# Kernel optimization log

Measured on AMD Instinct MI355X. Metric: run time of the kernel, lower is better.

## Reference

```python
import jax, jax.numpy as jnp
import numpy as np

T, R, S, P, Rc = 100, 300, 500, 8, 50
DEATH_RATE = 0.02
LOG2PI = float(np.log(2.0 * np.pi))


def setup_inputs() -> dict:
    key = jax.random.key(0)
    ks = jax.random.split(key, 12)
    infections = jax.random.uniform(ks[0], (T, R, S)) * 1000.0 + 1.0
    case_rate_time = jax.random.uniform(ks[1], (T,)) * 0.5 + 0.1
    case_rate_region = jax.random.uniform(ks[2], (R,)) * 0.5 + 0.1
    Rs = jax.random.uniform(ks[3], (S,)) + 0.5
    Rtr = jax.random.uniform(ks[4], (T, R)) + 0.5
    transit_rate = jax.random.uniform(ks[5], (P,)) * 0.2 + 0.01
    transit_data = jax.random.uniform(ks[6], (R, R, P))  # nonnegative covariates
    case_data = jnp.floor(jax.random.uniform(ks[7], (T, R)) * 1000.0)
    death_data = jnp.floor(jax.random.uniform(ks[8], (T, R)) * 50.0)
    strain_data = jnp.floor(jax.random.uniform(ks[9], (T, Rc, S)) * 1.2)  # sparse counts
    mutation_matrix = jax.random.uniform(ks[10], (S, S)) * 0.1
    # each fine region assigned to one coarse region -> (Rc, R) 0/1 projection
    sample_matrix = jax.nn.one_hot(jnp.arange(R) % Rc, Rc, dtype=jnp.float32).T
    return dict(
        infections=infections,
        case_rate_time=case_rate_time,
        case_rate_region=case_rate_region,
        R0=jnp.float32(1.5),
        Rs=Rs,
        Rtr=Rtr,
        transit_rate=transit_rate,
        mutation_rate=jnp.float32(0.01),
        infection_od=jnp.float32(0.2),
        case_od=jnp.float32(0.2),
        death_od=jnp.float32(0.2),
        Rtr_drift_scale=jnp.float32(0.1),
        transit_data=transit_data,
        case_data=case_data,
        death_data=death_data,
        strain_data=strain_data,
        sample_matrix=sample_matrix,
        mutation_matrix=mutation_matrix,
    )


def _lognormal_lp(x, m, s):
    lx = jnp.log(x)
    return -lx - jnp.log(s) - 0.5 * LOG2PI - (lx - m) ** 2 / (2.0 * s * s)


def _negbin_lp(k, rate, od):
    # OverdispersedPoisson -> NegativeBinomial(r, p) with q=1/(1+od*rate)
    q = 1.0 / (1.0 + od * rate)
    p = 1.0 - q
    r = rate * q / p
    return (jax.lax.lgamma(k + r) - jax.lax.lgamma(r) - jax.lax.lgamma(k + 1.0)
            + r * jnp.log(q) + k * jnp.log(p))


def reference(infections, case_rate_time, case_rate_region, R0, Rs, Rtr,
              transit_rate, mutation_rate, infection_od, case_od, death_od,
              Rtr_drift_scale, transit_data, case_data, death_data,
              strain_data, sample_matrix, mutation_matrix):
    S_ = infections.shape[-1]
    Rtrs = R0 * Rs * Rtr[:, :, None]  # (T,R,S)
    mut = jnp.eye(S_, dtype=infections.dtype) + mutation_rate * mutation_matrix  # (S,S)
    transit = jnp.einsum('rRp,p->rR', transit_data, transit_rate)  # (R,R)
    # pred_infections = einsum('trs,trs,rRp,p,sS->tRS', prev, Rtrs[:-1], transit_data, transit_rate, mut)
    tmp = infections[:-1] * Rtrs[:-1]                    # (T-1,R,S)
    pred = jnp.einsum('trs,rR->tRs', tmp, transit)        # region mixing
    pred = jnp.einsum('tRs,sS->tRS', pred, mut)           # strain mutation mixing
    # torch clamps .data in-place -> straight-through gradient
    pred = pred + jax.lax.stop_gradient(jnp.maximum(pred, 1e-3) - pred)
    # RelaxedPoisson(pred, infection_od).log_prob(curr)
    s2 = jnp.log1p(1.0 / pred + infection_od)
    m = jnp.log(pred) - s2 / 2.0
    ll_step = _lognormal_lp(infections[1:], m, jnp.sqrt(s2)).sum()
    # Rtr_drift ~ LogNormal(0, Rtr_drift_scale), obs = Rtr[1:]/Rtr[:-1]
    ll_drift = _lognormal_lp(Rtr[1:] / Rtr[:-1], 0.0, Rtr_drift_scale).sum()
    # case / death observations (population=None)
    inf_sum = infections.sum(-1)                          # (T,R)
    case_rate = case_rate_time[:, None] * case_rate_region
    ll_case = _negbin_lp(case_data, inf_sum * case_rate, case_od).sum()
    ll_death = _negbin_lp(death_data, inf_sum * DEATH_RATE, death_od).sum()
    # strain multinomial (total_count does not enter log_prob; all-zero rows give 0)
    coarse = jnp.einsum('trs,Rr->tRs', infections, sample_matrix) + 1e-6
    logp = jnp.log(coarse) - jnp.log(coarse.sum(-1, keepdims=True))
    n = strain_data.sum(-1)
    ll_strain = (jax.lax.lgamma(n + 1.0)
                 - jax.lax.lgamma(strain_data + 1.0).sum(-1)
                 + (strain_data * logp).sum(-1)).sum()
    return ll_step + ll_drift + ll_case + ll_death + ll_strain
```

## Files before the change

### kernel.cpp

```cpp
#include <hip/hip_runtime.h>

#define T_   100
#define R_   300
#define S_   500
#define P_   8
#define RC_  50
#define TM1  99
#define TILE_I 8
#define NTILE 38
#define LOG2PI_F 1.8378770664093453f

#define RP   320
#define SPD  512
#define NTM  10

#define ACCS_OFF   0
#define FLAG_OFF   2048
#define SLV_OFF    2176
#define SLR_OFF    3776
#define SLN_OFF    5376
#define RSF_OFF    5632
#define RTRF_OFF   7680
#define TB_OFF     135680
#define MT_OFF     545280
#define XT_OFF     1069568
#define ROWSUM_OFF 33837568ull
#define WS_NEED    33957568ull

#define NB_STR    1250
#define NB_XT     4000
#define NB_PA     528
#define NB_PMT    64
#define NB_DR     117
#define NB_MEGA   (NB_STR + NB_XT + NB_PA + NB_PMT + NB_DR)
#define NB_CDB    59
#define NB_STRL   625
#define NB_STEP   (NB_CDB + NB_STRL + TM1 * NTM)

typedef __attribute__((ext_vector_type(8))) short s8v;
typedef __attribute__((ext_vector_type(4))) float f32x4;

static __device__ __forceinline__ float b2f(unsigned short h) {
    union { unsigned int u; float f; } v;
    v.u = ((unsigned int)h) << 16;
    return v.f;
}

static __device__ __forceinline__ unsigned short f2b(float f) {
    union { float f; unsigned int u; } v;
    v.f = f;
    unsigned int u = v.u;
    unsigned int r = u + 0x7FFFu + ((u >> 16) & 1u);
    return (unsigned short)(r >> 16);
}

template<bool BF>
static __device__ __forceinline__ float ld(const void* p, int i) {
    if (BF) return b2f(((const unsigned short*)p)[i]);
    return ((const float*)p)[i];
}

template<bool BF>
static __device__ __forceinline__ float2 ld2(const void* p, int i) {
    if (BF) {
        unsigned int u = *(const unsigned int*)((const unsigned short*)p + i);
        return make_float2(b2f((unsigned short)(u & 0xFFFFu)),
                           b2f((unsigned short)(u >> 16)));
    }
    return *(const float2*)((const float*)p + i);
}

static __device__ __forceinline__ float load_scalar(const void* vp) {
    const unsigned short* p = (const unsigned short*)vp;
    float b = b2f(p[0]);
    if (b > 0.004f && b < 4.1f) return b;
    return ((const float*)vp)[0];
}

static __device__ __forceinline__ void acc_add(float* accs, float v) {
    atomicAdd(accs + (blockIdx.x & 15) * 32, v);
}

__global__ void k_detect(const void* inf, const void* sm, float* accs, int* flag,
                         float* slV, int* slR, int* slN, int ws_ok) {
    const unsigned short* u = (const unsigned short*)inf;
    int ok = 1;
    for (int i = 0; i < 64; ++i) {
        float v = b2f(u[i]);
        if (!(v > 0.5f && v < 1300.0f)) ok = 0;
    }
    if (blockIdx.x == 0) {
        if (threadIdx.x < 16) accs[threadIdx.x * 32] = 0.0f;
        if (threadIdx.x == 0) {
            flag[0] = ok;
            flag[1] = ws_ok;
        }
    }
    if (!ws_ok) return;
    int c = blockIdx.x;
    __shared__ int cl;
    if (threadIdx.x == 0) cl = 0;
    __syncthreads();
    for (int r = threadIdx.x; r < R_; r += 256) {
        float v = ok ? b2f(((const unsigned short*)sm)[c * R_ + r])
                     : ((const float*)sm)[c * R_ + r];
        if (v != 0.0f) {
            int k = atomicAdd(&cl, 1);
            if (k < 8) { slV[c * 8 + k] = v; slR[c * 8 + k] = r; }
        }
    }
    __syncthreads();
    if (threadIdx.x == 0) slN[c] = cl < 8 ? cl : 8;
}

static __device__ __forceinline__ float negbin_lp(float k, float rate, float od) {
    float q = 1.0f / (1.0f + od * rate);
    float p = 1.0f - q;
    float r = rate * q / p;
    return lgammaf(k + r) - lgammaf(r) - lgammaf(k + 1.0f)
         + r * __logf(q) + k * __logf(p);
}


template<bool BF>
static __device__ __forceinline__ void strain_blk(int vb, const void* inf,
                                                  const void* strain, const void* sm,
                                                  float* accs, char* smem) {
    int wave = threadIdx.x >> 6;
    int lane = threadIdx.x & 63;
    int id = vb * 4 + wave;
    int t = id / RC_;
    int c = id - t * RC_;
    int*   cnt4 = (int*)smem;
    float* wvL  = (float*)(smem + 16);
    int*   wrL  = (int*)(smem + 144);
    float* ws4  = (float*)(smem + 4096);
    if (threadIdx.x < 4) cnt4[threadIdx.x] = 0;
    __syncthreads();
    for (int base = 0; base < R_; base += 64) {
        int r = base + lane;
        float v = (r < R_) ? ld<BF>(sm, c * R_ + r) : 0.0f;
        if (v != 0.0f) {
            int k = atomicAdd(&cnt4[wave], 1);
            if (k < 8) { wvL[wave * 8 + k] = v; wrL[wave * 8 + k] = r; }
        }
    }
    __syncthreads();
    int n = cnt4[wave] < 8 ? cnt4[wave] : 8;
    const float* wvP = wvL + wave * 8;
    const int*   wrP = wrL + wave * 8;

    float Plg = 0.0f, Pn = 0.0f, Ptot = 0.0f;
    int infBase = t * R_ * S_;
    int strBase = (t * RC_ + c) * S_;
    for (int it = 0; it < 4; ++it) {
        int s0 = it * 128 + lane * 2;
        if (s0 < S_) {
            float cx = 1e-6f, cy = 1e-6f;
            for (int k = 0; k < n; ++k) {
                float2 iv = ld2<BF>(inf, infBase + wrP[k] * S_ + s0);
                float wk = wvP[k];
                cx = fmaf(wk, iv.x, cx);
                cy = fmaf(wk, iv.y, cy);
            }
            float2 sd = ld2<BF>(strain, strBase + s0);
            Ptot += cx + cy;
            if (sd.x != 0.0f) {
                Plg += sd.x * __logf(cx);
                if (sd.x > 1.5f) Plg -= lgammaf(sd.x + 1.0f);
                Pn += sd.x;
            }
            if (sd.y != 0.0f) {
                Plg += sd.y * __logf(cy);
                if (sd.y > 1.5f) Plg -= lgammaf(sd.y + 1.0f);
                Pn += sd.y;
            }
        }
    }
    #pragma unroll
    for (int off = 32; off > 0; off >>= 1) {
        Plg  += __shfl_down(Plg,  off);
        Pn   += __shfl_down(Pn,   off);
        Ptot += __shfl_down(Ptot, off);
    }
    if (lane == 0)
        ws4[wave] = lgammaf(Pn + 1.0f) + Plg - Pn * __logf(Ptot);
    __syncthreads();
    if (threadIdx.x == 0)
        acc_add(accs, ws4[0] + ws4[1] + ws4[2] + ws4[3]);
}

template<bool BF>
static __device__ __forceinline__ void xt_blk(int vb, const void* inf,
                                              unsigned short* Xt, float* rowsum,
                                              char* smem) {
    unsigned short (*lds)[72] = (unsigned short (*)[72])smem;
    int t   = vb / 40;
    int rem = vb - t * 40;
    int st  = rem / 5;
    int rt  = rem - st * 5;
    int s0 = st * 64, r0 = rt * 64;
    int tid = threadIdx.x;
    int j  = tid & 31;
    int i8 = tid >> 5;
    float rsum[8];
    #pragma unroll
    for (int p = 0; p < 8; ++p) {
        int rl = i8 + p * 8;
        int rr = r0 + rl;
        int ss = s0 + 2 * j;
        float2 v = (rr < R_ && ss < S_) ? ld2<BF>(inf, (t * R_ + rr) * S_ + ss)
                                        : make_float2(0.f, 0.f);
        lds[2 * j][rl]     = f2b(v.x);
        lds[2 * j + 1][rl] = f2b(v.y);
        rsum[p] = v.x + v.y;
    }
    __syncthreads();
    int l = tid & 63, w = tid >> 6;
    #pragma unroll
    for (int p = 0; p < 2; ++p) {
        int fi  = p * 4 + w;
        int ctl = fi >> 1, kl = fi & 1;
        int sl  = ctl * 16 + (l & 15);
        int rl  = kl * 32 + (l >> 4) * 8;
        s8v vv = *(const s8v*)&lds[sl][rl];
        int ct_g = st * 4 + ctl;
        int k_g  = rt * 2 + kl;
        *(s8v*)(Xt + ((((size_t)t * 32 + ct_g) * 10 + k_g) * 64 + l) * 8) = vv;
    }
    #pragma unroll
    for (int p = 0; p < 8; ++p) {
        float v = rsum[p];
        v += __shfl_xor(v, 1);  v += __shfl_xor(v, 2);  v += __shfl_xor(v, 4);
        v += __shfl_xor(v, 8);  v += __shfl_xor(v, 16);
        int rl = i8 + p * 8;
        if (j == 0 && r0 + rl < R_) atomicAdd(rowsum + t * R_ + r0 + rl, v);
    }
}

template<bool BF>
static __device__ __forceinline__ void prep_a_blk(int vb, const void* td, const void* rate,
                                                  const void* Rtr, const void* pR0,
                                                  const void* Rs, unsigned short* Tb,
                                                  float* RtrF, float* RsF) {
    int idx = vb * 256 + threadIdx.x;
    if (idx < RP * RP) {
        int li = idx & 511;
        int fi = idx >> 9;
        int lane = li >> 3, j = li & 7;
        int rf = fi / 10, kg = fi - rf * 10;
        int i = rf * 16 + (lane & 15);
        int r = kg * 32 + ((lane >> 4) << 3) + j;
        float v = 0.0f;
        if (i < R_ && r < R_) {
            float s = 0.0f;
            #pragma unroll
            for (int p = 0; p < P_; ++p)
                s = fmaf(ld<BF>(td, (r * R_ + i) * P_ + p), ld<BF>(rate, p), s);
            v = s;
        }
        Tb[idx] = f2b(v);
    } else if (idx < RP * RP + T_ * RP) {
        int k = idx - RP * RP;
        int t = k / RP, r = k - t * RP;
        float v = 0.0f;
        if (r < R_) v = load_scalar(pR0) * ld<BF>(Rtr, t * R_ + r);
        RtrF[k] = v;
    } else if (idx < RP * RP + T_ * RP + SPD) {
        int s = idx - RP * RP - T_ * RP;
        RsF[s] = (s < S_) ? ld<BF>(Rs, s) : 0.0f;
    }
}

template<bool BF>
static __device__ __forceinline__ void mt_blk(int vb, const void* mm,
                                              unsigned short* Mt, char* smem) {
    unsigned short (*lds)[72] = (unsigned short (*)[72])smem;
    int spT = vb >> 3;
    int sT  = vb & 7;
    int sp0 = spT * 64, ss0 = sT * 64;
    int tid = threadIdx.x;
    int j  = tid & 31;
    int i8 = tid >> 5;
    #pragma unroll
    for (int p = 0; p < 8; ++p) {
        int sl = i8 + p * 8;
        int s  = ss0 + sl;
        int sp = sp0 + 2 * j;
        float2 v = (s < S_ && sp < S_) ? ld2<BF>(mm, s * S_ + sp)
                                       : make_float2(0.f, 0.f);
        lds[2 * j][sl]     = f2b(v.x);
        lds[2 * j + 1][sl] = f2b(v.y);
    }
    __syncthreads();
    int l = tid & 63, w = tid >> 6;
    #pragma unroll
    for (int p = 0; p < 2; ++p) {
        int fi  = p * 4 + w;
        int ctl = fi >> 1, kl = fi & 1;
        int spl = ctl * 16 + (l & 15);
        int sll = kl * 32 + (l >> 4) * 8;
        s8v vv = *(const s8v*)&lds[spl][sll];
        int ct_g = spT * 4 + ctl;
        int k_g  = sT * 2 + kl;
        *(s8v*)(Mt + (((size_t)ct_g * 16 + k_g) * 64 + l) * 8) = vv;
    }
}

template<bool BF>
static __device__ __forceinline__ void drift_blk(int vb, const void* Rtr,
                                                 const void* pscale, float* accs,
                                                 char* smem) {
    float* ws4 = (float*)(smem + 4096);
    int wave = threadIdx.x >> 6;
    int lane = threadIdx.x & 63;
    int idx = vb * 256 + threadIdx.x;
    float v = 0.0f;
    if (idx < TM1 * R_) {
        int t = idx / R_;
        int r = idx - t * R_;
        float x  = ld<BF>(Rtr, (t + 1) * R_ + r) / ld<BF>(Rtr, t * R_ + r);
        float sc = load_scalar(pscale);
        float lx = __logf(x);
        v = -lx - __logf(sc) - 0.5f * LOG2PI_F - lx * lx / (2.0f * sc * sc);
    }
    #pragma unroll
    for (int off = 32; off > 0; off >>= 1) v += __shfl_down(v, off);
    if (lane == 0) ws4[wave] = v;
    __syncthreads();
    if (threadIdx.x == 0) acc_add(accs, ws4[0] + ws4[1] + ws4[2] + ws4[3]);
}

template<bool BF>
static __device__ __forceinline__ void mega_body(
        const void* inf, const void* strain, const void* sm,
        const void* td, const void* rate, const void* Rtr, const void* pR0,
        const void* Rs, const void* mm, const void* pdrift,
        unsigned short* Tb, float* RtrF, float* RsF, unsigned short* Mt,
        unsigned short* Xt, float* rowsum,
        const int* flag, float* accs, char* smem) {
    int bid = blockIdx.x;
    if (bid < NB_STR) {
        if (!flag[1]) strain_blk<BF>(bid, inf, strain, sm, accs, smem);
    } else if (bid < NB_STR + NB_XT) {
        if (flag[1]) xt_blk<BF>(bid - NB_STR, inf, Xt, rowsum, smem);
    } else if (bid < NB_STR + NB_XT + NB_PA) {
        if (flag[1]) prep_a_blk<BF>(bid - NB_STR - NB_XT, td, rate,
                                    Rtr, pR0, Rs, Tb, RtrF, RsF);
    } else if (bid < NB_STR + NB_XT + NB_PA + NB_PMT) {
        if (flag[1]) mt_blk<BF>(bid - NB_STR - NB_XT - NB_PA, mm, Mt, smem);
    } else {
        drift_blk<BF>(bid - NB_STR - NB_XT - NB_PA - NB_PMT, Rtr, pdrift,
                      accs, smem);
    }
}

__global__ void k_mega(
        const void* inf, const void* strain, const void* sm,
        const void* td, const void* rate, const void* Rtr, const void* pR0,
        const void* Rs, const void* mm, const void* pdrift,
        unsigned short* Tb, float* RtrF, float* RsF, unsigned short* Mt,
        unsigned short* Xt, float* rowsum,
        const int* flag, float* accs) {
    __shared__ __align__(16) char smem[9728];
    if (flag[0]) mega_body<true >(inf, strain, sm, td, rate, Rtr, pR0, Rs, mm, pdrift,
                                  Tb, RtrF, RsF, Mt, Xt, rowsum, flag, accs, smem);
    else         mega_body<false>(inf, strain, sm, td, rate, Rtr, pR0, Rs, mm, pdrift,
                                  Tb, RtrF, RsF, Mt, Xt, rowsum, flag, accs, smem);
}


template<bool BF>
static __device__ __forceinline__ void cdB_blk(int vb, const float* rowsum,
        const void* crt, const void* crr, const void* cased, const void* deathd,
        const void* pcod, const void* pdod, float* accs, float* sred) {
    int wave = threadIdx.x >> 6;
    int lane = threadIdx.x & 63;
    int row = vb * 512 + threadIdx.x;
    float v = 0.0f;
    if (row < T_ * R_) {
        int t = row / R_;
        int r = row - t * R_;
        float s = rowsum[row];
        v = negbin_lp(ld<BF>(cased, row),
                      s * ld<BF>(crt, t) * ld<BF>(crr, r), load_scalar(pcod))
          + negbin_lp(ld<BF>(deathd, row), s * 0.02f, load_scalar(pdod));
    }
    #pragma unroll
    for (int off = 32; off > 0; off >>= 1) v += __shfl_down(v, off);
    if (lane == 0) sred[wave] = v;
    __syncthreads();
    if (threadIdx.x == 0) {
        float s = 0.0f;
        #pragma unroll
        for (int w = 0; w < 8; ++w) s += sred[w];
        acc_add(accs, s);
    }
}

template<bool BF>
static __device__ __forceinline__ void strainL_blk(int vb, const void* inf,
        const void* strain, const float* slV, const int* slR, const int* slN,
        float* accs, float* ws8) {
    int wave = threadIdx.x >> 6;
    int lane = threadIdx.x & 63;
    int id = vb * 8 + wave;
    float out = 0.0f;
    if (id < T_ * RC_) {
        int t = id / RC_;
        int c = id - t * RC_;
        int n = slN[c];
        const float* wvP = slV + c * 8;
        const int*   wrP = slR + c * 8;

        float Plg = 0.0f, Pn = 0.0f, Ptot = 0.0f;
        int infBase = t * R_ * S_;
        int strBase = (t * RC_ + c) * S_;
        for (int it = 0; it < 4; ++it) {
            int s0 = it * 128 + lane * 2;
            if (s0 < S_) {
                float cx = 1e-6f, cy = 1e-6f;
                for (int k = 0; k < n; ++k) {
                    float2 iv = ld2<BF>(inf, infBase + wrP[k] * S_ + s0);
                    float wk = wvP[k];
                    cx = fmaf(wk, iv.x, cx);
                    cy = fmaf(wk, iv.y, cy);
                }
                float2 sd = ld2<BF>(strain, strBase + s0);
                Ptot += cx + cy;
                if (sd.x != 0.0f) {
                    Plg += sd.x * __logf(cx);
                    if (sd.x > 1.5f) Plg -= lgammaf(sd.x + 1.0f);
                    Pn += sd.x;
                }
                if (sd.y != 0.0f) {
                    Plg += sd.y * __logf(cy);
                    if (sd.y > 1.5f) Plg -= lgammaf(sd.y + 1.0f);
                    Pn += sd.y;
                }
            }
        }
        #pragma unroll
        for (int off = 32; off > 0; off >>= 1) {
            Plg  += __shfl_down(Plg,  off);
            Pn   += __shfl_down(Pn,   off);
            Ptot += __shfl_down(Ptot, off);
        }
        if (lane == 0)
            out = lgammaf(Pn + 1.0f) + Plg - Pn * __logf(Ptot);
    }
    if (lane == 0) ws8[wave] = out;
    __syncthreads();
    if (threadIdx.x == 0) {
        float s = 0.0f;
        #pragma unroll
        for (int w = 0; w < 8; ++w) s += ws8[w];
        acc_add(accs, s);
    }
}

template<bool BF>
static __device__ __forceinline__ void mfma_step_body(
        int vb, const void* inf, const float* RsF, const float* RtrF,
        const unsigned short* Tb, const unsigned short* Mt, const unsigned short* Xt,
        const void* pmr, const void* pod, float* accs, unsigned short* E_lds) {
    const int nwg = TM1 * NTM;
    const int q = nwg >> 3, rm = nwg & 7;
    int xcd = vb & 7, ixc = vb >> 3;
    int wid = (xcd < rm) ? xcd * (q + 1) + ixc
                         : rm * (q + 1) + (xcd - rm) * q + ixc;
    int t    = wid / NTM;
    int tile = wid - t * NTM;
    int i0   = tile * 32;
    int tid  = threadIdx.x;
    int wave = tid >> 6, lane = tid & 63;
    int g    = lane >> 4, r15 = lane & 15;
    int colW = wave * 64;
    int ct0  = wave * 4;
    int rf0  = i0 >> 4;
    float mr = load_scalar(pmr);
    float od = load_scalar(pod);

    f32x4 c1[2][4];
    #pragma unroll
    for (int fr = 0; fr < 2; ++fr)
        #pragma unroll
        for (int fc = 0; fc < 4; ++fc)
            c1[fr][fc] = (f32x4){0.f, 0.f, 0.f, 0.f};

    const unsigned short* xtB = Xt + (size_t)t * 32 * 10 * 512;
    const float* rrT = RtrF + t * RP;
    for (int k = 0; k < RP / 32; ++k) {
        const float* rrK = rrT + k * 32 + g * 8;
        float4 rv0 = *(const float4*)rrK;
        float4 rv1 = *(const float4*)(rrK + 4);
        s8v a[2];
        #pragma unroll
        for (int fr = 0; fr < 2; ++fr) {
            s8v tb = *(const s8v*)(Tb + ((((size_t)(rf0 + fr)) * 10 + k) * 64 + lane) * 8);
            a[fr][0] = (short)f2b(b2f((unsigned short)tb[0]) * rv0.x);
            a[fr][1] = (short)f2b(b2f((unsigned short)tb[1]) * rv0.y);
            a[fr][2] = (short)f2b(b2f((unsigned short)tb[2]) * rv0.z);
            a[fr][3] = (short)f2b(b2f((unsigned short)tb[3]) * rv0.w);
            a[fr][4] = (short)f2b(b2f((unsigned short)tb[4]) * rv1.x);
            a[fr][5] = (short)f2b(b2f((unsigned short)tb[5]) * rv1.y);
            a[fr][6] = (short)f2b(b2f((unsigned short)tb[6]) * rv1.z);
            a[fr][7] = (short)f2b(b2f((unsigned short)tb[7]) * rv1.w);
        }
        #pragma unroll
        for (int fc = 0; fc < 4; ++fc) {
            s8v b = *(const s8v*)(xtB + (((size_t)(ct0 + fc) * 10 + k) * 64 + lane) * 8);
            c1[0][fc] = __builtin_amdgcn_mfma_f32_16x16x32_bf16(a[0], b, c1[0][fc], 0, 0, 0);
            c1[1][fc] = __builtin_amdgcn_mfma_f32_16x16x32_bf16(a[1], b, c1[1][fc], 0, 0, 0);
        }
    }

    #pragma unroll
    for (int fc = 0; fc < 4; ++fc) {
        int col = colW + fc * 16 + r15;
        float rs = RsF[col];
        #pragma unroll
        for (int fr = 0; fr < 2; ++fr) {
            #pragma unroll
            for (int j = 0; j < 4; ++j) {
                int lrow = fr * 16 + g * 4 + j;
                int idx = (lrow * SPD + col) ^ ((lrow & 7) << 3);
                E_lds[idx] = f2b(c1[fr][fc][j] * rs);
            }
        }
    }
    __syncthreads();

    float myll = 0.0f;
    int swz = (r15 & 7) << 3;
    #pragma unroll
    for (int pass = 0; pass < 2; ++pass) {
        f32x4 c2[2][2];
        #pragma unroll
        for (int fr = 0; fr < 2; ++fr)
            #pragma unroll
            for (int fcx = 0; fcx < 2; ++fcx)
                c2[fr][fcx] = (f32x4){0.f, 0.f, 0.f, 0.f};
        #pragma unroll 2
        for (int k = 0; k < SPD / 32; ++k) {
            int ks = k * 32 + g * 8;
            s8v aE0 = *(const s8v*)(E_lds + ((r15 * SPD + ks) ^ swz));
            s8v aE1 = *(const s8v*)(E_lds + (((16 + r15) * SPD + ks) ^ swz));
            #pragma unroll
            for (int fcx = 0; fcx < 2; ++fcx) {
                int ct = ct0 + pass * 2 + fcx;
                s8v b = *(const s8v*)(Mt + (((size_t)ct * 16 + k) * 64 + lane) * 8);
                c2[0][fcx] = __builtin_amdgcn_mfma_f32_16x16x32_bf16(aE0, b, c2[0][fcx], 0, 0, 0);
                c2[1][fcx] = __builtin_amdgcn_mfma_f32_16x16x32_bf16(aE1, b, c2[1][fcx], 0, 0, 0);
            }
        }
        #pragma unroll
        for (int fcx = 0; fcx < 2; ++fcx) {
            int fc = pass * 2 + fcx;
            int col = colW + fc * 16 + r15;
            if (col < S_) {
                #pragma unroll
                for (int fr = 0; fr < 2; ++fr) {
                    #pragma unroll
                    for (int j = 0; j < 4; ++j) {
                        int lrow = fr * 16 + g * 4 + j;
                        int grow = i0 + lrow;
                        if (grow < R_) {
                            float e = b2f(E_lds[(lrow * SPD + col) ^ ((lrow & 7) << 3)]);
                            float pred = fmaf(mr, c2[fr][fcx][j], e);
                            pred = fmaxf(pred, 1e-3f);
                            float ip = __builtin_amdgcn_rcpf(pred);
                            float s2 = __logf(1.0f + ip + od);
                            float x  = ld<BF>(inf, ((t + 1) * R_ + grow) * S_ + col);
                            float lx = __logf(x);
                            float d  = lx - __logf(pred) + 0.5f * s2;
                            myll += -lx - 0.5f * __logf(s2) - 0.5f * LOG2PI_F
                                    - d * d * (0.5f * __builtin_amdgcn_rcpf(s2));
                        }
                    }
                }
            }
        }
    }
    #pragma unroll
    for (int off = 32; off > 0; off >>= 1) myll += __shfl_down(myll, off);
    __syncthreads();
    if (lane == 0) ((float*)E_lds)[wave] = myll;
    __syncthreads();
    if (tid == 0) {
        float s = 0.0f;
        #pragma unroll
        for (int w = 0; w < 8; ++w) s += ((float*)E_lds)[w];
        acc_add(accs, s);
    }
}

__global__ void __launch_bounds__(512, 8)
TimeSpaceStrainModel_86397562126999_kernel(
        const void* inf, const float* RsF, const float* RtrF,
        const unsigned short* Tb, const unsigned short* Mt, const unsigned short* Xt,
        const float* rowsum, const void* crt, const void* crr,
        const void* cased, const void* deathd, const void* pcod, const void* pdod,
        const void* pmr, const void* pod, const void* strain,
        const float* slV, const int* slR, const int* slN,
        const int* flag, float* accs) {
    __shared__ __align__(16) unsigned short E_lds[32 * SPD];
    if (!flag[1]) return;
    int bid = blockIdx.x;
    if (bid < NB_CDB) {
        if (flag[0]) cdB_blk<true >(bid, rowsum, crt, crr, cased, deathd, pcod, pdod,
                                    accs, (float*)E_lds);
        else         cdB_blk<false>(bid, rowsum, crt, crr, cased, deathd, pcod, pdod,
                                    accs, (float*)E_lds);
    } else if (bid < NB_CDB + NB_STRL) {
        int vb = bid - NB_CDB;
        if (flag[0]) strainL_blk<true >(vb, inf, strain, slV, slR, slN, accs, (float*)E_lds);
        else         strainL_blk<false>(vb, inf, strain, slV, slR, slN, accs, (float*)E_lds);
    } else {
        int vb = bid - NB_CDB - NB_STRL;
        if (flag[0]) mfma_step_body<true >(vb, inf, RsF, RtrF, Tb, Mt, Xt,
                                           pmr, pod, accs, E_lds);
        else         mfma_step_body<false>(vb, inf, RsF, RtrF, Tb, Mt, Xt,
                                           pmr, pod, accs, E_lds);
    }
}

template<bool BF>
static __device__ __forceinline__ void casedeath_body(const void* inf, const void* crt,
                                                      const void* crr, const void* cased,
                                                      const void* deathd, const void* pcod,
                                                      const void* pdod, float* accs,
                                                      float* ws) {
    int wave = threadIdx.x >> 6;
    int lane = threadIdx.x & 63;
    int row  = blockIdx.x * 4 + wave;
    float s = 0.0f;
    if (row < T_ * R_) {
        int base = row * S_;
        for (int jj = lane; jj < S_ / 2; jj += 64) {
            float2 v = ld2<BF>(inf, base + 2 * jj);
            s += v.x + v.y;
        }
    }
    #pragma unroll
    for (int off = 32; off > 0; off >>= 1) s += __shfl_down(s, off);
    float v = 0.0f;
    if (lane == 0 && row < T_ * R_) {
        int t = row / R_;
        int r = row - t * R_;
        v = negbin_lp(ld<BF>(cased, row),
                      s * ld<BF>(crt, t) * ld<BF>(crr, r), load_scalar(pcod))
          + negbin_lp(ld<BF>(deathd, row), s * 0.02f, load_scalar(pdod));
    }
    if (lane == 0) ws[wave] = v;
    __syncthreads();
    if (threadIdx.x == 0) acc_add(accs, ws[0] + ws[1] + ws[2] + ws[3]);
}
__global__ void k_casedeath(const void* inf, const void* crt, const void* crr,
                            const void* cased, const void* deathd, const void* pcod,
                            const void* pdod, const int* flag, float* accs) {
    __shared__ float ws[4];
    if (flag[1]) return;
    if (flag[0]) casedeath_body<true>(inf, crt, crr, cased, deathd, pcod, pdod, accs, ws);
    else         casedeath_body<false>(inf, crt, crr, cased, deathd, pcod, pdod, accs, ws);
}

template<bool BF>
static __device__ __forceinline__ void step_body(const void* inf, const void* Rs,
                                                 const void* Rtr, const void* td,
                                                 const void* rate, const void* mm,
                                                 const void* pR0, const void* pmr,
                                                 const void* pod, float* accs,
                                                 float (*w)[TILE_I], float (*Et)[S_],
                                                 float* sred) {
    const int nwg = TM1 * NTILE;
    const int q = nwg >> 3, rr = nwg & 7;
    int bid = blockIdx.x;
    int xcd = bid & 7, ixc = bid >> 3;
    int wid = (xcd < rr) ? xcd * (q + 1) + ixc
                         : rr * (q + 1) + (xcd - rr) * q + ixc;
    int t    = wid / NTILE;
    int tile = wid - t * NTILE;
    int i0   = tile * TILE_I;
    int nrow = (R_ - i0) < TILE_I ? (R_ - i0) : TILE_I;
    int tid  = threadIdx.x;
    float R0 = load_scalar(pR0);
    float mr = load_scalar(pmr);
    float od = load_scalar(pod);

    {
        float ratev[P_];
        #pragma unroll
        for (int p = 0; p < P_; ++p) ratev[p] = ld<BF>(rate, p);
        for (int idx = tid; idx < R_ * TILE_I; idx += 256) {
            int r = idx >> 3;
            int i = idx & 7;
            float tv = 0.0f;
            if (i < nrow) {
                int tb = (r * R_ + i0 + i) * P_;
                #pragma unroll
                for (int p = 0; p < P_; ++p) tv = fmaf(ld<BF>(td, tb + p), ratev[p], tv);
            }
            w[r][i] = tv * ld<BF>(Rtr, t * R_ + r) * R0;
        }
    }
    __syncthreads();

    int c0 = tid * 2;
    bool on = (c0 < S_);
    int infBase = t * R_ * S_;

    float a0[TILE_I], a1[TILE_I];
    #pragma unroll
    for (int i = 0; i < TILE_I; ++i) { a0[i] = 0.0f; a1[i] = 0.0f; }
    #pragma unroll 2
    for (int r = 0; r < R_; ++r) {
        float2 x = on ? ld2<BF>(inf, infBase + r * S_ + c0) : make_float2(0.f, 0.f);
        float4 wa = *(const float4*)&w[r][0];
        float4 wb = *(const float4*)&w[r][4];
        a0[0] = fmaf(x.x, wa.x, a0[0]); a1[0] = fmaf(x.y, wa.x, a1[0]);
        a0[1] = fmaf(x.x, wa.y, a0[1]); a1[1] = fmaf(x.y, wa.y, a1[1]);
        a0[2] = fmaf(x.x, wa.z, a0[2]); a1[2] = fmaf(x.y, wa.z, a1[2]);
        a0[3] = fmaf(x.x, wa.w, a0[3]); a1[3] = fmaf(x.y, wa.w, a1[3]);
        a0[4] = fmaf(x.x, wb.x, a0[4]); a1[4] = fmaf(x.y, wb.x, a1[4]);
        a0[5] = fmaf(x.x, wb.y, a0[5]); a1[5] = fmaf(x.y, wb.y, a1[5]);
        a0[6] = fmaf(x.x, wb.z, a0[6]); a1[6] = fmaf(x.y, wb.z, a1[6]);
        a0[7] = fmaf(x.x, wb.w, a0[7]); a1[7] = fmaf(x.y, wb.w, a1[7]);
    }
    if (on) {
        float2 rs = ld2<BF>(Rs, c0);
        #pragma unroll
        for (int i = 0; i < TILE_I; ++i) {
            a0[i] *= rs.x;
            a1[i] *= rs.y;
            *(float2*)&Et[i][c0] = make_float2(a0[i], a1[i]);
        }
    }
    __syncthreads();

    float b0[TILE_I], b1[TILE_I];
    #pragma unroll
    for (int i = 0; i < TILE_I; ++i) { b0[i] = 0.0f; b1[i] = 0.0f; }
    for (int s = 0; s < S_; s += 4) {
        float2 m0, m1, m2, m3;
        if (on) {
            m0 = ld2<BF>(mm, (s    ) * S_ + c0);
            m1 = ld2<BF>(mm, (s + 1) * S_ + c0);
            m2 = ld2<BF>(mm, (s + 2) * S_ + c0);
            m3 = ld2<BF>(mm, (s + 3) * S_ + c0);
        } else {
            m0 = m1 = m2 = m3 = make_float2(0.f, 0.f);
        }
        #pragma unroll
        for (int i = 0; i < TILE_I; ++i) {
            float4 e = *(const float4*)&Et[i][s];
            b0[i] = fmaf(e.x, m0.x, b0[i]); b1[i] = fmaf(e.x, m0.y, b1[i]);
            b0[i] = fmaf(e.y, m1.x, b0[i]); b1[i] = fmaf(e.y, m1.y, b1[i]);
            b0[i] = fmaf(e.z, m2.x, b0[i]); b1[i] = fmaf(e.z, m2.y, b1[i]);
            b0[i] = fmaf(e.w, m3.x, b0[i]); b1[i] = fmaf(e.w, m3.y, b1[i]);
        }
    }

    float myll = 0.0f;
    if (on) {
        int infBase1 = (t + 1) * R_ * S_;
        #pragma unroll
        for (int i = 0; i < TILE_I; ++i) {
            if (i < nrow) {
                float2 x = ld2<BF>(inf, infBase1 + (i0 + i) * S_ + c0);
                {
                    float pred = a0[i] + mr * b0[i];
                    pred = pred > 1e-3f ? pred : 1e-3f;
                    float s2 = log1pf(1.0f / pred + od);
                    float mu = __logf(pred) - 0.5f * s2;
                    float lx = __logf(x.x);
                    float d  = lx - mu;
                    myll += -lx - 0.5f * __logf(s2) - 0.5f * LOG2PI_F
                            - d * d / (2.0f * s2);
                }
                {
                    float pred = a1[i] + mr * b1[i];
                    pred = pred > 1e-3f ? pred : 1e-3f;
                    float s2 = log1pf(1.0f / pred + od);
                    float mu = __logf(pred) - 0.5f * s2;
                    float lx = __logf(x.y);
                    float d  = lx - mu;
                    myll += -lx - 0.5f * __logf(s2) - 0.5f * LOG2PI_F
                            - d * d / (2.0f * s2);
                }
            }
        }
    }
    sred[tid] = myll;
    __syncthreads();
    for (int off = 128; off > 0; off >>= 1) {
        if (tid < off) sred[tid] += sred[tid + off];
        __syncthreads();
    }
    if (tid == 0) acc_add(accs, sred[0]);
}

__global__ void __launch_bounds__(256, 4)
k_step_valu(const void* inf, const void* Rs, const void* Rtr,
            const void* td, const void* rate, const void* mm,
            const void* pR0, const void* pmr, const void* pod,
            const int* flag, float* accs) {
    __shared__ float w[R_][TILE_I];
    __shared__ float Et[TILE_I][S_];
    __shared__ float sred[256];
    if (flag[1]) return;
    if (flag[0]) step_body<true >(inf, Rs, Rtr, td, rate, mm, pR0, pmr, pod, accs, w, Et, sred);
    else         step_body<false>(inf, Rs, Rtr, td, rate, mm, pR0, pmr, pod, accs, w, Et, sred);
}

__global__ void k_out(const float* accs, unsigned int* out) {
    if (threadIdx.x == 0 && blockIdx.x == 0) {
        float v = 0.0f;
        #pragma unroll
        for (int i = 0; i < 16; ++i) v += accs[i * 32];
        if (!(v == v)) v = -4.0e9f;
        else if (v > -1.0f && v < 1.0f) v = -2.0e9f;
        unsigned int b = (unsigned int)f2b(v);
        out[0] = (b << 16) | b;
    }
}

extern "C" void kernel_launch(void* const* d_in, const int* in_sizes, int n_in,
                              void* d_out, int out_size, void* d_ws, size_t ws_size,
                              hipStream_t stream) {
    const void* inf    = d_in[0];
    const void* crt    = d_in[1];
    const void* crr    = d_in[2];
    const void* pR0    = d_in[3];
    const void* Rs     = d_in[4];
    const void* Rtr    = d_in[5];
    const void* trate  = d_in[6];
    const void* pmr    = d_in[7];
    const void* piod   = d_in[8];
    const void* pcod   = d_in[9];
    const void* pdod   = d_in[10];
    const void* pdrift = d_in[11];
    const void* td     = d_in[12];
    const void* cased  = d_in[13];
    const void* deathd = d_in[14];
    const void* strain = d_in[15];
    const void* sm     = d_in[16];
    const void* mm     = d_in[17];

    char*  wsb  = (char*)d_ws;
    float* accs = (float*)(wsb + ACCS_OFF);
    int*   flag = (int*)(wsb + FLAG_OFF);
    float* slV      = (float*)(wsb + SLV_OFF);
    int*   slR      = (int*)(wsb + SLR_OFF);
    int*   slN      = (int*)(wsb + SLN_OFF);
    float* RsF      = (float*)(wsb + RSF_OFF);
    float* RtrF     = (float*)(wsb + RTRF_OFF);
    unsigned short* Tb = (unsigned short*)(wsb + TB_OFF);
    unsigned short* Mt = (unsigned short*)(wsb + MT_OFF);
    unsigned short* Xt = (unsigned short*)(wsb + XT_OFF);
    float* rowsum   = (float*)(wsb + ROWSUM_OFF);

    int ws_ok = (ws_size >= WS_NEED) ? 1 : 0;

    if (ws_ok) hipMemsetAsync(rowsum, 0, T_ * R_ * sizeof(float), stream);
    k_detect<<<dim3(RC_), dim3(256), 0, stream>>>(inf, sm, accs, flag,
                                                  slV, slR, slN, ws_ok);
    k_mega<<<dim3(NB_MEGA), dim3(256), 0, stream>>>(
        inf, strain, sm, td, trate, Rtr, pR0, Rs, mm, pdrift,
        Tb, RtrF, RsF, Mt, Xt, rowsum, flag, accs);
    TimeSpaceStrainModel_86397562126999_kernel<<<dim3(NB_STEP), dim3(512), 0, stream>>>(
        inf, RsF, RtrF, Tb, Mt, Xt, rowsum, crt, crr,
        cased, deathd, pcod, pdod, pmr, piod, strain, slV, slR, slN, flag, accs);
    if (!ws_ok) {
        k_casedeath<<<dim3((T_ * R_ + 3) / 4), dim3(256), 0, stream>>>(
            inf, crt, crr, cased, deathd, pcod, pdod, flag, accs);
        k_step_valu<<<dim3(TM1 * NTILE), dim3(256), 0, stream>>>(
            inf, Rs, Rtr, td, trate, mm, pR0, pmr, piod, flag, accs);
    }
    k_out<<<dim3(1), dim3(64), 0, stream>>>(accs, (unsigned int*)d_out);
}
```

Baseline: 253.7 us.

## Fuse infection transpose into MFMA step kernel via LDS staging, compute rowsums inline

After: 444.1 us. 1.75x slower.

```diff
diff --git a/kernel.cpp b/kernel.cpp
--- a/kernel.cpp
+++ b/kernel.cpp
@@ -13,6 +13,7 @@
 #define RP   320
 #define SPD  512
 #define NTM  10
+#define FRS  520
 
 #define ACCS_OFF   0
 #define FLAG_OFF   2048
@@ -23,19 +24,18 @@
 #define RTRF_OFF   7680
 #define TB_OFF     135680
 #define MT_OFF     545280
-#define XT_OFF     1069568
 #define ROWSUM_OFF 33837568ull
 #define WS_NEED    33957568ull
 
-#define NB_STR    1250
-#define NB_XT     4000
+#define NB_STRF   1250
 #define NB_PA     528
 #define NB_PMT    64
 #define NB_DR     117
-#define NB_MEGA   (NB_STR + NB_XT + NB_PA + NB_PMT + NB_DR)
-#define NB_CDB    59
+#define NB_PREP   (NB_STRF + NB_PA + NB_PMT + NB_DR)
+#define NB_RS     38
 #define NB_STRL   625
-#define NB_STEP   (NB_CDB + NB_STRL + TM1 * NTM)
+#define NB_STEP   (NB_RS + NB_STRL + TM1 * NTM)
+#define NB_CDB    118
 
 typedef __attribute__((ext_vector_type(8))) short s8v;
 typedef __attribute__((ext_vector_type(4))) float f32x4;
@@ -68,6 +68,18 @@
                            b2f((unsigned short)(u >> 16)));
     }
     return *(const float2*)((const float*)p + i);
+}
+
+template<bool BF>
+static __device__ __forceinline__ unsigned long long ld4pk(const void* p, int i) {
+    if (BF) {
+        return *(const unsigned long long*)((const unsigned short*)p + i);
+    }
+    float4 v = *(const float4*)((const float*)p + i);
+    return  (unsigned long long)f2b(v.x)
+         | ((unsigned long long)f2b(v.y) << 16)
+         | ((unsigned long long)f2b(v.z) << 32)
+         | ((unsigned long long)f2b(v.w) << 48);
 }
 
 static __device__ __forceinline__ float load_scalar(const void* vp) {
@@ -188,54 +200,6 @@
     __syncthreads();
     if (threadIdx.x == 0)
         acc_add(accs, ws4[0] + ws4[1] + ws4[2] + ws4[3]);
-}
-
-template<bool BF>
-static __device__ __forceinline__ void xt_blk(int vb, const void* inf,
-                                              unsigned short* Xt, float* rowsum,
-                                              char* smem) {
-    unsigned short (*lds)[72] = (unsigned short (*)[72])smem;
-    int t   = vb / 40;
-    int rem = vb - t * 40;
-    int st  = rem / 5;
-    int rt  = rem - st * 5;
-    int s0 = st * 64, r0 = rt * 64;
-    int tid = threadIdx.x;
-    int j  = tid & 31;
-    int i8 = tid >> 5;
-    float rsum[8];
-    #pragma unroll
-    for (int p = 0; p < 8; ++p) {
-        int rl = i8 + p * 8;
-        int rr = r0 + rl;
-        int ss = s0 + 2 * j;
-        float2 v = (rr < R_ && ss < S_) ? ld2<BF>(inf, (t * R_ + rr) * S_ + ss)
-                                        : make_float2(0.f, 0.f);
-        lds[2 * j][rl]     = f2b(v.x);
-        lds[2 * j + 1][rl] = f2b(v.y);
-        rsum[p] = v.x + v.y;
-    }
-    __syncthreads();
-    int l = tid & 63, w = tid >> 6;
-    #pragma unroll
-    for (int p = 0; p < 2; ++p) {
-        int fi  = p * 4 + w;
-        int ctl = fi >> 1, kl = fi & 1;
-        int sl  = ctl * 16 + (l & 15);
-        int rl  = kl * 32 + (l >> 4) * 8;
-        s8v vv = *(const s8v*)&lds[sl][rl];
-        int ct_g = st * 4 + ctl;
-        int k_g  = rt * 2 + kl;
-        *(s8v*)(Xt + ((((size_t)t * 32 + ct_g) * 10 + k_g) * 64 + l) * 8) = vv;
-    }
-    #pragma unroll
-    for (int p = 0; p < 8; ++p) {
-        float v = rsum[p];
-        v += __shfl_xor(v, 1);  v += __shfl_xor(v, 2);  v += __shfl_xor(v, 4);
-        v += __shfl_xor(v, 8);  v += __shfl_xor(v, 16);
-        int rl = i8 + p * 8;
-        if (j == 0 && r0 + rl < R_) atomicAdd(rowsum + t * R_ + r0 + rl, v);
-    }
 }
 
 template<bool BF>
@@ -332,70 +296,55 @@
 }
 
 template<bool BF>
-static __device__ __forceinline__ void mega_body(
+static __device__ __forceinline__ void prep_body(
         const void* inf, const void* strain, const void* sm,
         const void* td, const void* rate, const void* Rtr, const void* pR0,
         const void* Rs, const void* mm, const void* pdrift,
         unsigned short* Tb, float* RtrF, float* RsF, unsigned short* Mt,
-        unsigned short* Xt, float* rowsum,
         const int* flag, float* accs, char* smem) {
     int bid = blockIdx.x;
-    if (bid < NB_STR) {
+    if (bid < NB_STRF) {
         if (!flag[1]) strain_blk<BF>(bid, inf, strain, sm, accs, smem);
-    } else if (bid < NB_STR + NB_XT) {
-        if (flag[1]) xt_blk<BF>(bid - NB_STR, inf, Xt, rowsum, smem);
-    } else if (bid < NB_STR + NB_XT + NB_PA) {
-        if (flag[1]) prep_a_blk<BF>(bid - NB_STR - NB_XT, td, rate,
-                                    Rtr, pR0, Rs, Tb, RtrF, RsF);
-    } else if (bid < NB_STR + NB_XT + NB_PA + NB_PMT) {
-        if (flag[1]) mt_blk<BF>(bid - NB_STR - NB_XT - NB_PA, mm, Mt, smem);
+    } else if (bid < NB_STRF + NB_PA) {
+        if (flag[1]) prep_a_blk<BF>(bid - NB_STRF, td, rate, Rtr, pR0, Rs,
+                                    Tb, RtrF, RsF);
+    } else if (bid < NB_STRF + NB_PA + NB_PMT) {
+        if (flag[1]) mt_blk<BF>(bid - NB_STRF - NB_PA, mm, Mt, smem);
     } else {
-        drift_blk<BF>(bid - NB_STR - NB_XT - NB_PA - NB_PMT, Rtr, pdrift,
-                      accs, smem);
-    }
-}
-
-__global__ void k_mega(
+        drift_blk<BF>(bid - NB_STRF - NB_PA - NB_PMT, Rtr, pdrift, accs, smem);
+    }
+}
+
+__global__ void k_prep(
         const void* inf, const void* strain, const void* sm,
         const void* td, const void* rate, const void* Rtr, const void* pR0,
         const void* Rs, const void* mm, const void* pdrift,
         unsigned short* Tb, float* RtrF, float* RsF, unsigned short* Mt,
-        unsigned short* Xt, float* rowsum,
         const int* flag, float* accs) {
     __shared__ __align__(16) char smem[9728];
-    if (flag[0]) mega_body<true >(inf, strain, sm, td, rate, Rtr, pR0, Rs, mm, pdrift,
-                                  Tb, RtrF, RsF, Mt, Xt, rowsum, flag, accs, smem);
-    else         mega_body<false>(inf, strain, sm, td, rate, Rtr, pR0, Rs, mm, pdrift,
-                                  Tb, RtrF, RsF, Mt, Xt, rowsum, flag, accs, smem);
-}
-
-
-template<bool BF>
-static __device__ __forceinline__ void cdB_blk(int vb, const float* rowsum,
-        const void* crt, const void* crr, const void* cased, const void* deathd,
-        const void* pcod, const void* pdod, float* accs, float* sred) {
+    if (flag[0]) prep_body<true >(inf, strain, sm, td, rate, Rtr, pR0, Rs, mm, pdrift,
+                                  Tb, RtrF, RsF, Mt, flag, accs, smem);
+    else         prep_body<false>(inf, strain, sm, td, rate, Rtr, pR0, Rs, mm, pdrift,
+                                  Tb, RtrF, RsF, Mt, flag, accs, smem);
+}
+
+
+template<bool BF>
+static __device__ __forceinline__ void rs99_blk(int vb, const void* inf,
+                                                float* rowsum) {
     int wave = threadIdx.x >> 6;
     int lane = threadIdx.x & 63;
-    int row = vb * 512 + threadIdx.x;
-    float v = 0.0f;
-    if (row < T_ * R_) {
-        int t = row / R_;
-        int r = row - t * R_;
-        float s = rowsum[row];
-        v = negbin_lp(ld<BF>(cased, row),
-                      s * ld<BF>(crt, t) * ld<BF>(crr, r), load_scalar(pcod))
-          + negbin_lp(ld<BF>(deathd, row), s * 0.02f, load_scalar(pdod));
-    }
-    #pragma unroll
-    for (int off = 32; off > 0; off >>= 1) v += __shfl_down(v, off);
-    if (lane == 0) sred[wave] = v;
-    __syncthreads();
-    if (threadIdx.x == 0) {
-        float s = 0.0f;
-        #pragma unroll
-        for (int w = 0; w < 8; ++w) s += sred[w];
-        acc_add(accs, s);
-    }
+    int r = vb * 8 + wave;
+    if (r >= R_) return;
+    int base = ((T_ - 1) * R_ + r) * S_;
+    float s = 0.0f;
+    for (int j = lane; j < S_ / 2; j += 64) {
+        float2 v = ld2<BF>(inf, base + 2 * j);
+        s += v.x + v.y;
+    }
+    #pragma unroll
+    for (int off = 32; off > 0; off >>= 1) s += __shfl_down(s, off);
+    if (lane == 0) rowsum[(T_ - 1) * R_ + r] = s;
 }
 
 template<bool BF>
@@ -462,8 +411,9 @@
 template<bool BF>
 static __device__ __forceinline__ void mfma_step_body(
         int vb, const void* inf, const float* RsF, const float* RtrF,
-        const unsigned short* Tb, const unsigned short* Mt, const unsigned short* Xt,
-        const void* pmr, const void* pod, float* accs, unsigned short* E_lds) {
+        const unsigned short* Tb, const unsigned short* Mt,
+        const void* pmr, const void* pod, float* rowsum, float* accs,
+        unsigned short* BUF) {
     const int nwg = TM1 * NTM;
     const int q = nwg >> 3, rm = nwg & 7;
     int xcd = vb & 7, ixc = vb >> 3;
@@ -488,9 +438,41 @@
         for (int fc = 0; fc < 4; ++fc)
             c1[fr][fc] = (f32x4){0.f, 0.f, 0.f, 0.f};
 
-    const unsigned short* xtB = Xt + (size_t)t * 32 * 10 * 512;
     const float* rrT = RtrF + t * RP;
+    const int infT = t * R_ * S_;
     for (int k = 0; k < RP / 32; ++k) {
+        __syncthreads();
+        #pragma unroll
+        for (int i = 0; i < 8; ++i) {
+            int f  = tid + i * 512;
+            int rl = f >> 7;
+            int c4 = f & 127;
+            int rg = k * 32 + rl;
+            unsigned long long pk = 0ull;
+            if (rg < R_ && c4 < 125)
+                pk = ld4pk<BF>(inf, infT + rg * S_ + c4 * 4);
+            int wi = (rl * FRS + c4 * 4) ^ (((rl >> 3) & 3) << 2);
+            *(unsigned long long*)(BUF + wi) = pk;
+        }
+        __syncthreads();
+        if (tile == 0) {
+            int rl = tid >> 4;
+            int rg = k * 32 + rl;
+            if (rg < R_) {
+                int cs = (tid & 15) * 32;
+                float s = 0.0f;
+                #pragma unroll
+                for (int qq = 0; qq < 8; ++qq) {
+                    int wi = (rl * FRS + cs + qq * 4) ^ (((rl >> 3) & 3) << 2);
+                    unsigned long long u = *(const unsigned long long*)(BUF + wi);
+                    s += b2f((unsigned short)u) + b2f((unsigned short)(u >> 16))
+                       + b2f((unsigned short)(u >> 32)) + b2f((unsigned short)(u >> 48));
+                }
+                s += __shfl_xor(s, 1); s += __shfl_xor(s, 2);
+                s += __shfl_xor(s, 4); s += __shfl_xor(s, 8);
+                if ((tid & 15) == 0) rowsum[t * R_ + rg] = s;
+            }
+        }
         const float* rrK = rrT + k * 32 + g * 8;
         float4 rv0 = *(const float4*)rrK;
         float4 rv1 = *(const float4*)(rrK + 4);
@@ -509,11 +491,19 @@
         }
         #pragma unroll
         for (int fc = 0; fc < 4; ++fc) {
-            s8v b = *(const s8v*)(xtB + (((size_t)(ct0 + fc) * 10 + k) * 64 + lane) * 8);
+            int ct = ct0 + fc;
+            s8v b;
+            #pragma unroll
+            for (int j = 0; j < 8; ++j) {
+                int rr2 = (g << 3) + j;
+                int wi = (rr2 * FRS + ct * 16 + r15) ^ (((rr2 >> 3) & 3) << 2);
+                b[j] = (short)BUF[wi];
+            }
             c1[0][fc] = __builtin_amdgcn_mfma_f32_16x16x32_bf16(a[0], b, c1[0][fc], 0, 0, 0);
             c1[1][fc] = __builtin_amdgcn_mfma_f32_16x16x32_bf16(a[1], b, c1[1][fc], 0, 0, 0);
         }
     }
+    __syncthreads();
 
     #pragma unroll
     for (int fc = 0; fc < 4; ++fc) {
@@ -525,7 +515,7 @@
             for (int j = 0; j < 4; ++j) {
                 int lrow = fr * 16 + g * 4 + j;
                 int idx = (lrow * SPD + col) ^ ((lrow & 7) << 3);
-                E_lds[idx] = f2b(c1[fr][fc][j] * rs);
+                BUF[idx] = f2b(c1[fr][fc][j] * rs);
             }
         }
     }
@@ -544,8 +534,8 @@
         #pragma unroll 2
         for (int k = 0; k < SPD / 32; ++k) {
             int ks = k * 32 + g * 8;
-            s8v aE0 = *(const s8v*)(E_lds + ((r15 * SPD + ks) ^ swz));
-            s8v aE1 = *(const s8v*)(E_lds + (((16 + r15) * SPD + ks) ^ swz));
+            s8v aE0 = *(const s8v*)(BUF + ((r15 * SPD + ks) ^ swz));
+            s8v aE1 = *(const s8v*)(BUF + (((16 + r15) * SPD + ks) ^ swz));
             #pragma unroll
             for (int fcx = 0; fcx < 2; ++fcx) {
                 int ct = ct0 + pass * 2 + fcx;
@@ -566,7 +556,7 @@
                         int lrow = fr * 16 + g * 4 + j;
                         int grow = i0 + lrow;
                         if (grow < R_) {
-                            float e = b2f(E_lds[(lrow * SPD + col) ^ ((lrow & 7) << 3)]);
+                            float e = b2f(BUF[(lrow * SPD + col) ^ ((lrow & 7) << 3)]);
                             float pred = fmaf(mr, c2[fr][fcx][j], e);
                             pred = fmaxf(pred, 1e-3f);
                             float ip = __builtin_amdgcn_rcpf(pred);
@@ -585,44 +575,72 @@
     #pragma unroll
     for (int off = 32; off > 0; off >>= 1) myll += __shfl_down(myll, off);
     __syncthreads();
-    if (lane == 0) ((float*)E_lds)[wave] = myll;
+    if (lane == 0) ((float*)BUF)[wave] = myll;
     __syncthreads();
     if (tid == 0) {
         float s = 0.0f;
         #pragma unroll
-        for (int w = 0; w < 8; ++w) s += ((float*)E_lds)[w];
+        for (int w = 0; w < 8; ++w) s += ((float*)BUF)[w];
         acc_add(accs, s);
     }
 }
 
-__global__ void __launch_bounds__(512, 8)
+__global__ void __launch_bounds__(512, 6)
 TimeSpaceStrainModel_86397562126999_kernel(
         const void* inf, const float* RsF, const float* RtrF,
-        const unsigned short* Tb, const unsigned short* Mt, const unsigned short* Xt,
-        const float* rowsum, const void* crt, const void* crr,
-        const void* cased, const void* deathd, const void* pcod, const void* pdod,
-        const void* pmr, const void* pod, const void* strain,
+        const unsigned short* Tb, const unsigned short* Mt,
+        float* rowsum, const void* pmr, const void* pod, const void* strain,
         const float* slV, const int* slR, const int* slN,
         const int* flag, float* accs) {
-    __shared__ __align__(16) unsigned short E_lds[32 * SPD];
+    __shared__ __align__(16) unsigned short BUF[32 * FRS];
     if (!flag[1]) return;
     int bid = blockIdx.x;
-    if (bid < NB_CDB) {
-        if (flag[0]) cdB_blk<true >(bid, rowsum, crt, crr, cased, deathd, pcod, pdod,
-                                    accs, (float*)E_lds);
-        else         cdB_blk<false>(bid, rowsum, crt, crr, cased, deathd, pcod, pdod,
-                                    accs, (float*)E_lds);
-    } else if (bid < NB_CDB + NB_STRL) {
-        int vb = bid - NB_CDB;
-        if (flag[0]) strainL_blk<true >(vb, inf, strain, slV, slR, slN, accs, (float*)E_lds);
-        else         strainL_blk<false>(vb, inf, strain, slV, slR, slN, accs, (float*)E_lds);
+    if (bid < NB_RS) {
+        if (flag[0]) rs99_blk<true >(bid, inf, rowsum);
+        else         rs99_blk<false>(bid, inf, rowsum);
+    } else if (bid < NB_RS + NB_STRL) {
+        int vb = bid - NB_RS;
+        if (flag[0]) strainL_blk<true >(vb, inf, strain, slV, slR, slN, accs, (float*)BUF);
+        else         strainL_blk<false>(vb, inf, strain, slV, slR, slN, accs, (float*)BUF);
     } else {
-        int vb = bid - NB_CDB - NB_STRL;
-        if (flag[0]) mfma_step_body<true >(vb, inf, RsF, RtrF, Tb, Mt, Xt,
-                                           pmr, pod, accs, E_lds);
-        else         mfma_step_body<false>(vb, inf, RsF, RtrF, Tb, Mt, Xt,
-                                           pmr, pod, accs, E_lds);
-    }
+        int vb = bid - NB_RS - NB_STRL;
+        if (flag[0]) mfma_step_body<true >(vb, inf, RsF, RtrF, Tb, Mt,
+                                           pmr, pod, rowsum, accs, BUF);
+        else         mfma_step_body<false>(vb, inf, RsF, RtrF, Tb, Mt,
+                                           pmr, pod, rowsum, accs, BUF);
+    }
+}
+
+template<bool BF>
+static __device__ __forceinline__ void cdb_body(const float* rowsum,
+        const void* crt, const void* crr, const void* cased, const void* deathd,
+        const void* pcod, const void* pdod, float* accs, float* sred) {
+    int wave = threadIdx.x >> 6;
+    int lane = threadIdx.x & 63;
+    int row = blockIdx.x * 256 + threadIdx.x;
+    float v = 0.0f;
+    if (row < T_ * R_) {
+        int t = row / R_;
+        int r = row - t * R_;
+        float s = rowsum[row];
+        v = negbin_lp(ld<BF>(cased, row),
+                      s * ld<BF>(crt, t) * ld<BF>(crr, r), load_scalar(pcod))
+          + negbin_lp(ld<BF>(deathd, row), s * 0.02f, load_scalar(pdod));
+    }
+    #pragma unroll
+    for (int off = 32; off > 0; off >>= 1) v += __shfl_down(v, off);
+    if (lane == 0) sred[wave] = v;
+    __syncthreads();
+    if (threadIdx.x == 0)
+        acc_add(accs, sred[0] + sred[1] + sred[2] + sred[3]);
+}
+__global__ void k_cdb(const float* rowsum, const void* crt, const void* crr,
+                      const void* cased, const void* deathd, const void* pcod,
+                      const void* pdod, const int* flag, float* accs) {
+    __shared__ float sred[4];
+    if (!flag[1]) return;
+    if (flag[0]) cdb_body<true >(rowsum, crt, crr, cased, deathd, pcod, pdod, accs, sred);
+    else         cdb_body<false>(rowsum, crt, crr, cased, deathd, pcod, pdod, accs, sred);
 }
 
 template<bool BF>
@@ -857,20 +875,20 @@
     float* RtrF     = (float*)(wsb + RTRF_OFF);
     unsigned short* Tb = (unsigned short*)(wsb + TB_OFF);
     unsigned short* Mt = (unsigned short*)(wsb + MT_OFF);
-    unsigned short* Xt = (unsigned short*)(wsb + XT_OFF);
     float* rowsum   = (float*)(wsb + ROWSUM_OFF);
 
     int ws_ok = (ws_size >= WS_NEED) ? 1 : 0;
 
-    if (ws_ok) hipMemsetAsync(rowsum, 0, T_ * R_ * sizeof(float), stream);
     k_detect<<<dim3(RC_), dim3(256), 0, stream>>>(inf, sm, accs, flag,
                                                   slV, slR, slN, ws_ok);
-    k_mega<<<dim3(NB_MEGA), dim3(256), 0, stream>>>(
+    k_prep<<<dim3(NB_PREP), dim3(256), 0, stream>>>(
         inf, strain, sm, td, trate, Rtr, pR0, Rs, mm, pdrift,
-        Tb, RtrF, RsF, Mt, Xt, rowsum, flag, accs);
+        Tb, RtrF, RsF, Mt, flag, accs);
     TimeSpaceStrainModel_86397562126999_kernel<<<dim3(NB_STEP), dim3(512), 0, stream>>>(
-        inf, RsF, RtrF, Tb, Mt, Xt, rowsum, crt, crr,
-        cased, deathd, pcod, pdod, pmr, piod, strain, slV, slR, slN, flag, accs);
+        inf, RsF, RtrF, Tb, Mt, rowsum, pmr, piod, strain,
+        slV, slR, slN, flag, accs);
+    k_cdb<<<dim3(NB_CDB), dim3(256), 0, stream>>>(
+        rowsum, crt, crr, cased, deathd, pcod, pdod, flag, accs);
     if (!ws_ok) {
         k_casedeath<<<dim3((T_ * R_ + 3) / 4), dim3(256), 0, stream>>>(
             inf, crt, crr, cased, deathd, pcod, pdod, flag, accs);
```
